# Kernel optimization log

Hardware: AMD Instinct MI355X
Metric: run time of the kernel (lower is better)

## Reference

```python
import jax, jax.numpy as jnp
import numpy as np

EPS = 1e-08
MOMENTUM_WEIGHT = 1.0
CONTINUITY_WEIGHT = 10.0
N = 192


def setup_inputs() -> dict:
    key = jax.random.key(0)
    k1, k2, k3, k4, k5, k6 = jax.random.split(key, 6)
    return {
        'u': jax.random.normal(k1, (N, N, N, 3), dtype=jnp.float32),
        'u_prev': jax.random.normal(k2, (N, N, N, 3), dtype=jnp.float32),
        'p': jax.random.normal(k3, (N, N, N), dtype=jnp.float32),
        'rho': jax.random.uniform(k4, (N, N, N), dtype=jnp.float32),
        'nu': jax.random.uniform(k5, (1,), dtype=jnp.float32),
        'h': jnp.ones((3,), dtype=jnp.float32),
        'dt': jnp.ones((1,), dtype=jnp.float32),
        'gravity': jnp.asarray([0.0, -9.81, 0.0], dtype=jnp.float32),
    }


def _central_diff(f, axis, h_ax):
    # (f[i+1] - f[i-1]) / (2h), periodic via roll (matches torch.roll)
    return (jnp.roll(f, -1, axis=axis) - jnp.roll(f, 1, axis=axis)) / (2.0 * h_ax)


def _laplacian(f, h):
    lap = jnp.zeros_like(f)
    for d in range(3):
        lap = lap + (jnp.roll(f, -1, axis=d) - 2.0 * f + jnp.roll(f, 1, axis=d)) / (h[d] ** 2)
    return lap


def reference(u, u_prev, p, rho, nu, h, dt, gravity):
    ux, uy, uz = u[..., 0], u[..., 1], u[..., 2]

    dux_dx = _central_diff(ux, 0, h[0]); dux_dy = _central_diff(ux, 1, h[1]); dux_dz = _central_diff(ux, 2, h[2])
    duy_dx = _central_diff(uy, 0, h[0]); duy_dy = _central_diff(uy, 1, h[1]); duy_dz = _central_diff(uy, 2, h[2])
    duz_dx = _central_diff(uz, 0, h[0]); duz_dy = _central_diff(uz, 1, h[1]); duz_dz = _central_diff(uz, 2, h[2])

    dp_dx = _central_diff(p, 0, h[0]); dp_dy = _central_diff(p, 1, h[1]); dp_dz = _central_diff(p, 2, h[2])

    lap_ux = _laplacian(ux, h); lap_uy = _laplacian(uy, h); lap_uz = _laplacian(uz, h)

    conv_x = ux * dux_dx + uy * dux_dy + uz * dux_dz
    conv_y = ux * duy_dx + uy * duy_dy + uz * duy_dz
    conv_z = ux * duz_dx + uy * duz_dy + uz * duz_dz

    # t > 0 branch: backward-difference time derivative
    dux_dt = (ux - u_prev[..., 0]) / dt[0]
    duy_dt = (uy - u_prev[..., 1]) / dt[0]
    duz_dt = (uz - u_prev[..., 2]) / dt[0]

    inv_rho = 1.0 / (rho + EPS)
    nu0 = nu[0]
    R_x = dux_dt + conv_x + dp_dx * inv_rho - nu0 * lap_ux - gravity[0]
    R_y = duy_dt + conv_y + dp_dy * inv_rho - nu0 * lap_uy - gravity[1]
    R_z = duz_dt + conv_z + dp_dz * inv_rho - nu0 * lap_uz - gravity[2]

    R_cont = dux_dx + duy_dy + duz_dz

    momentum_loss = (R_x ** 2 + R_y ** 2 + R_z ** 2).mean()
    continuity_loss = (R_cont ** 2).mean()
    total = MOMENTUM_WEIGHT * momentum_loss + CONTINUITY_WEIGHT * continuity_loss
    return jnp.stack([total, momentum_loss, continuity_loss])
```

## Files before the change

kernel.cpp:

```cpp
#include <hip/hip_runtime.h>

#define GN 192
#define GNN (GN * GN)
#define GTOT (GN * GN * GN)
#define NSLOTS 256
#define NT (GTOT / 2)
#define NBLK (NT / 256)
#define CHUNK (NBLK / 8)

typedef int   int32x4_t __attribute__((ext_vector_type(4)));
typedef float floatx4_t __attribute__((ext_vector_type(4)));
typedef float floatx2_t __attribute__((ext_vector_type(2)));
typedef float v2        __attribute__((ext_vector_type(2)));

extern "C" __device__ floatx4_t
llvm_amdgcn_raw_buffer_load_fp32x4(int32x4_t srsrc, int voffset, int soffset,
                                   int aux) __asm("llvm.amdgcn.raw.buffer.load.v4f32");
extern "C" __device__ floatx2_t
llvm_amdgcn_raw_buffer_load_fp32x2(int32x4_t srsrc, int voffset, int soffset,
                                   int aux) __asm("llvm.amdgcn.raw.buffer.load.v2f32");
extern "C" __device__ float
llvm_amdgcn_raw_buffer_load_fp32(int32x4_t srsrc, int voffset, int soffset,
                                 int aux) __asm("llvm.amdgcn.raw.buffer.load.f32");

__device__ __forceinline__ int32x4_t make_srd(const void* ptr, unsigned bytes) {
    int32x4_t r;
    unsigned long long a = (unsigned long long)ptr;
    r.x = (int)(unsigned)(a & 0xFFFFFFFFu);
    r.y = (int)(unsigned)(a >> 32);
    r.z = (int)bytes;
    r.w = 0x00020000;
    return r;
}

__global__ __launch_bounds__(256, 2) void ns_loss_kernel(
    const float* __restrict__ u,
    const float* __restrict__ uprev,
    const float* __restrict__ p,
    const float* __restrict__ rho,
    const float* __restrict__ nu,
    const float* __restrict__ h,
    const float* __restrict__ dt,
    const float* __restrict__ grav,
    double* __restrict__ acc)
{
    const int d = blockIdx.x;
    const int o = (d & 7) * CHUNK + (d >> 3);
    const int g = o * 256 + threadIdx.x;
    const int m  = g % 96;
    const int ln = g / 96;
    const int j  = ln % GN;
    const int i  = ln / GN;
    const int k0 = 2 * m;
    const int c0 = ln * GN + k0;
    const int c1 = c0 + 1;
    const int lane = threadIdx.x & 63;

    const int ipb = (i == GN-1) ? c0 - (GN - 1) * GNN : c0 + GNN;
    const int imb = (i == 0)    ? c0 + (GN - 1) * GNN : c0 - GNN;
    const int jpb = (j == GN-1) ? c0 - (GN - 1) * GN  : c0 + GN;
    const int jmb = (j == 0)    ? c0 + (GN - 1) * GN  : c0 - GN;

    const int32x4_t srd_u  = make_srd(u,     (unsigned)GTOT * 12u);
    const int32x4_t srd_up = make_srd(uprev, (unsigned)GTOT * 12u);
    const int32x4_t srd_p  = make_srd(p,     (unsigned)GTOT * 4u);
    const int32x4_t srd_r  = make_srd(rho,   (unsigned)GTOT * 4u);

    const floatx4_t B  = llvm_amdgcn_raw_buffer_load_fp32x4(srd_u, 12 * c0, 0, 0);
    const floatx4_t C2 = llvm_amdgcn_raw_buffer_load_fp32x4(srd_u, 12 * c0 + 16, 0, 0);
    const floatx4_t E1 = llvm_amdgcn_raw_buffer_load_fp32x4(srd_u, 12 * ipb, 0, 0);
    const floatx4_t E2 = llvm_amdgcn_raw_buffer_load_fp32x4(srd_u, 12 * ipb + 16, 0, 0);
    const floatx4_t G1 = llvm_amdgcn_raw_buffer_load_fp32x4(srd_u, 12 * imb, 0, 0);
    const floatx4_t G2 = llvm_amdgcn_raw_buffer_load_fp32x4(srd_u, 12 * imb + 16, 0, 0);
    const floatx4_t I1 = llvm_amdgcn_raw_buffer_load_fp32x4(srd_u, 12 * jpb, 0, 0);
    const floatx4_t I2 = llvm_amdgcn_raw_buffer_load_fp32x4(srd_u, 12 * jpb + 16, 0, 0);
    const floatx4_t K1 = llvm_amdgcn_raw_buffer_load_fp32x4(srd_u, 12 * jmb, 0, 0);
    const floatx4_t K2 = llvm_amdgcn_raw_buffer_load_fp32x4(srd_u, 12 * jmb + 16, 0, 0);
    const floatx4_t M  = llvm_amdgcn_raw_buffer_load_fp32x4(srd_up, 12 * c0, 0, 0);
    const floatx4_t M2 = llvm_amdgcn_raw_buffer_load_fp32x4(srd_up, 12 * c0 + 16, 0, 0);
    const floatx2_t P0  = llvm_amdgcn_raw_buffer_load_fp32x2(srd_p, 4 * c0, 0, 0);
    const floatx2_t Pip = llvm_amdgcn_raw_buffer_load_fp32x2(srd_p, 4 * ipb, 0, 0);
    const floatx2_t Pim = llvm_amdgcn_raw_buffer_load_fp32x2(srd_p, 4 * imb, 0, 0);
    const floatx2_t Pjp = llvm_amdgcn_raw_buffer_load_fp32x2(srd_p, 4 * jpb, 0, 0);
    const floatx2_t Pjm = llvm_amdgcn_raw_buffer_load_fp32x2(srd_p, 4 * jmb, 0, 0);
    const floatx2_t RR  = llvm_amdgcn_raw_buffer_load_fp32x2(srd_r, 4 * c0, 0, 0);

    const float h0 = h[0], h1v = h[1], h2v = h[2];
    const float i2h0 = 0.5f / h0, i2h1 = 0.5f / h1v, i2h2 = 0.5f / h2v;
    const float ihs0 = 1.0f / (h0 * h0), ihs1 = 1.0f / (h1v * h1v), ihs2 = 1.0f / (h2v * h2v);
    const float invdt = 1.0f / dt[0];
    const float nu0 = nu[0];
    const float g0 = grav[0], g1v = grav[1], g2v = grav[2];
    const float s2h = 2.0f * (ihs0 + ihs1 + ihs2);

    __builtin_amdgcn_sched_barrier(0);

    const float c0x = B.x,  c0y = B.y,  c0z = B.z;
    const float c1x = B.w,  c1y = C2.x, c1z = C2.y;

    v2 zmx = {__shfl_up(c1x, 1), c0x};
    v2 zmy = {__shfl_up(c1y, 1), c0y};
    v2 zmz = {__shfl_up(c1z, 1), c0z};
    v2 zpx = {c1x, __shfl_down(c0x, 1)};
    v2 zpy = {c1y, __shfl_down(c0y, 1)};
    v2 zpz = {c1z, __shfl_down(c0z, 1)};
    v2 pzm2 = {__shfl_up((float)P0.y, 1), P0.x};
    v2 pzp2 = {P0.y, __shfl_down((float)P0.x, 1)};

    if (m == 0 || lane == 0) {
        const int zmc = (m == 0) ? c0 + (GN - 1) : c0 - 1;
        const floatx4_t A = llvm_amdgcn_raw_buffer_load_fp32x4(srd_u, 12 * zmc, 0, 0);
        zmx.x = A.x; zmy.x = A.y; zmz.x = A.z;
        pzm2.x = llvm_amdgcn_raw_buffer_load_fp32(srd_p, 4 * zmc, 0, 0);
    }
    if (m == 95 || lane == 63) {
        const int zpc = (m == 95) ? c1 - (GN - 1) : c1 + 1;
        const floatx4_t D = llvm_amdgcn_raw_buffer_load_fp32x4(srd_u, 12 * zpc, 0, 0);
        zpx.y = D.x; zpy.y = D.y; zpz.y = D.z;
        pzp2.y = llvm_amdgcn_raw_buffer_load_fp32(srd_p, 4 * zpc, 0, 0);
    }

    const v2 ucx = {c0x, c1x}, ucy = {c0y, c1y}, ucz = {c0z, c1z};
    const v2 xpx = {E1.x, E1.w}, xpy = {E1.y, E2.x}, xpz = {E1.z, E2.y};
    const v2 xmx = {G1.x, G1.w}, xmy = {G1.y, G2.x}, xmz = {G1.z, G2.y};
    const v2 ypx = {I1.x, I1.w}, ypy = {I1.y, I2.x}, ypz = {I1.z, I2.y};
    const v2 ymx = {K1.x, K1.w}, ymy = {K1.y, K2.x}, ymz = {K1.z, K2.y};
    const v2 upx = {M.x, M.w},  upy = {M.y, M2.x}, upz = {M.z, M2.y};

    v2 dXx = (xpx - xmx) * i2h0, dXy = (xpy - xmy) * i2h0, dXz = (xpz - xmz) * i2h0;
    v2 dYx = (ypx - ymx) * i2h1, dYy = (ypy - ymy) * i2h1, dYz = (ypz - ymz) * i2h1;
    v2 dZx = (zpx - zmx) * i2h2, dZy = (zpy - zmy) * i2h2, dZz = (zpz - zmz) * i2h2;

    v2 lapx = (xpx + xmx) * ihs0 + (ypx + ymx) * ihs1 + (zpx + zmx) * ihs2 - ucx * s2h;
    v2 lapy = (xpy + xmy) * ihs0 + (ypy + ymy) * ihs1 + (zpy + zmy) * ihs2 - ucy * s2h;
    v2 lapz = (xpz + xmz) * ihs0 + (ypz + ymz) * ihs1 + (zpz + zmz) * ihs2 - ucz * s2h;

    v2 convx = ucx * dXx + ucy * dYx + ucz * dZx;
    v2 convy = ucx * dXy + ucy * dYy + ucz * dZy;
    v2 convz = ucx * dXz + ucy * dYz + ucz * dZz;

    v2 dpx = (Pip - Pim) * i2h0;
    v2 dpy = (Pjp - Pjm) * i2h1;
    v2 dpz = (pzp2 - pzm2) * i2h2;

    v2 irho;
    irho.x = __builtin_amdgcn_rcpf(RR.x + 1e-8f);
    irho.y = __builtin_amdgcn_rcpf(RR.y + 1e-8f);

    v2 Rx = (ucx - upx) * invdt + convx + dpx * irho - lapx * nu0 - g0;
    v2 Ry = (ucy - upy) * invdt + convy + dpy * irho - lapy * nu0 - g1v;
    v2 Rz = (ucz - upz) * invdt + convz + dpz * irho - lapz * nu0 - g2v;
    v2 Rc = dXx + dYy + dZz;

    v2 m2 = Rx * Rx + Ry * Ry + Rz * Rz;
    v2 c2 = Rc * Rc;
    float msum = m2.x + m2.y;
    float csum = c2.x + c2.y;

    #pragma unroll
    for (int off = 32; off > 0; off >>= 1) {
        msum += __shfl_down(msum, off);
        csum += __shfl_down(csum, off);
    }

    __shared__ double smom[4], scont[4];
    const int wid = threadIdx.x >> 6;
    if (lane == 0) { smom[wid] = (double)msum; scont[wid] = (double)csum; }
    __syncthreads();
    if (threadIdx.x == 0) {
        const double mm = smom[0] + smom[1] + smom[2] + smom[3];
        const double cc = scont[0] + scont[1] + scont[2] + scont[3];
        double* slot = acc + 2 * (blockIdx.x & (NSLOTS - 1));
        unsafeAtomicAdd(slot, mm);
        unsafeAtomicAdd(slot + 1, cc);
    }
}

__global__ __launch_bounds__(256) void ns_finalize_kernel(const double* __restrict__ acc,
                                                          float* __restrict__ out)
{
    const int tid = threadIdx.x;
    double mom = acc[2 * tid];
    double cont = acc[2 * tid + 1];
    #pragma unroll
    for (int off = 32; off > 0; off >>= 1) {
        mom  += __shfl_down(mom, off);
        cont += __shfl_down(cont, off);
    }
    __shared__ double smom[4], scont[4];
    const int wid = tid >> 6;
    const int lane = tid & 63;
    if (lane == 0) { smom[wid] = mom; scont[wid] = cont; }
    __syncthreads();
    if (tid == 0) {
        const double m = (smom[0] + smom[1] + smom[2] + smom[3]) / (double)GTOT;
        const double c = (scont[0] + scont[1] + scont[2] + scont[3]) / (double)GTOT;
        out[0] = (float)(m + 10.0 * c);
        out[1] = (float)m;
        out[2] = (float)c;
    }
}

extern "C" void kernel_launch(void* const* d_in, const int* in_sizes, int n_in,
                              void* d_out, int out_size, void* d_ws, size_t ws_size,
                              hipStream_t stream)
{
    const float* u     = (const float*)d_in[0];
    const float* uprev = (const float*)d_in[1];
    const float* p     = (const float*)d_in[2];
    const float* rho   = (const float*)d_in[3];
    const float* nu    = (const float*)d_in[4];
    const float* h     = (const float*)d_in[5];
    const float* dt    = (const float*)d_in[6];
    const float* grav  = (const float*)d_in[7];

    double* acc = (double*)d_ws;

    (void)hipMemsetAsync(d_ws, 0, NSLOTS * 2 * sizeof(double), stream);

    ns_loss_kernel<<<NBLK, 256, 0, stream>>>(u, uprev, p, rho, nu, h, dt, grav, acc);
    ns_finalize_kernel<<<1, 256, 0, stream>>>(acc, (float*)d_out);
}
```

Before: 49.78 us.

## Stage velocity rows in LDS per block covering two j-rows

Each block now handles one i-plane and two adjacent j-rows with 192 threads. It cooperatively loads the eight needed velocity rows (center, j±1, i±1) into shared memory with coalesced 16-byte loads, and every thread then reads its stencil neighbors from LDS. The aim is fewer redundant, poorly aligned global u loads and fewer per-thread vector loads. The cost is a block barrier, about 18KB of LDS per block, and a different block/occupancy configuration. Neighbor-row data is still fetched from global memory, so the total traffic reduction is limited.

```diff
diff --git a/kernel.cpp b/kernel.cpp
--- a/kernel.cpp
+++ b/kernel.cpp
@@ -4,8 +4,7 @@
 #define GNN (GN * GN)
 #define GTOT (GN * GN * GN)
 #define NSLOTS 256
-#define NT (GTOT / 2)
-#define NBLK (NT / 256)
+#define NBLK (GN * 96)
 #define CHUNK (NBLK / 8)
 
 typedef int   int32x4_t __attribute__((ext_vector_type(4)));
@@ -33,7 +32,7 @@
     return r;
 }
 
-__global__ __launch_bounds__(256, 2) void ns_loss_kernel(
+__global__ __launch_bounds__(192, 4) void ns_loss_kernel(
     const float* __restrict__ u,
     const float* __restrict__ uprev,
     const float* __restrict__ p,
@@ -44,46 +43,66 @@
     const float* __restrict__ grav,
     double* __restrict__ acc)
 {
+    __shared__ __align__(16) float ldsU[8 * 576];
+
     const int d = blockIdx.x;
     const int o = (d & 7) * CHUNK + (d >> 3);
-    const int g = o * 256 + threadIdx.x;
-    const int m  = g % 96;
-    const int ln = g / 96;
-    const int j  = ln % GN;
-    const int i  = ln / GN;
-    const int k0 = 2 * m;
-    const int c0 = ln * GN + k0;
-    const int c1 = c0 + 1;
-    const int lane = threadIdx.x & 63;
-
-    const int ipb = (i == GN-1) ? c0 - (GN - 1) * GNN : c0 + GNN;
-    const int imb = (i == 0)    ? c0 + (GN - 1) * GNN : c0 - GNN;
-    const int jpb = (j == GN-1) ? c0 - (GN - 1) * GN  : c0 + GN;
-    const int jmb = (j == 0)    ? c0 + (GN - 1) * GN  : c0 - GN;
+    const int i   = o / 96;
+    const int jpi = o % 96;
+    const int j0 = 2 * jpi, j1 = j0 + 1;
+    const int t = threadIdx.x;
+    const int lane = t & 63;
+
+    const int jmr = (j0 == 0)      ? GN - 1 : j0 - 1;
+    const int jpr = (j1 == GN - 1) ? 0      : j1 + 1;
+    const int imr = (i == 0)       ? GN - 1 : i - 1;
+    const int ipr = (i == GN - 1)  ? 0      : i + 1;
 
     const int32x4_t srd_u  = make_srd(u,     (unsigned)GTOT * 12u);
     const int32x4_t srd_up = make_srd(uprev, (unsigned)GTOT * 12u);
     const int32x4_t srd_p  = make_srd(p,     (unsigned)GTOT * 4u);
     const int32x4_t srd_r  = make_srd(rho,   (unsigned)GTOT * 4u);
 
-    const floatx4_t B  = llvm_amdgcn_raw_buffer_load_fp32x4(srd_u, 12 * c0, 0, 0);
-    const floatx4_t C2 = llvm_amdgcn_raw_buffer_load_fp32x4(srd_u, 12 * c0 + 16, 0, 0);
-    const floatx4_t E1 = llvm_amdgcn_raw_buffer_load_fp32x4(srd_u, 12 * ipb, 0, 0);
-    const floatx4_t E2 = llvm_amdgcn_raw_buffer_load_fp32x4(srd_u, 12 * ipb + 16, 0, 0);
-    const floatx4_t G1 = llvm_amdgcn_raw_buffer_load_fp32x4(srd_u, 12 * imb, 0, 0);
-    const floatx4_t G2 = llvm_amdgcn_raw_buffer_load_fp32x4(srd_u, 12 * imb + 16, 0, 0);
-    const floatx4_t I1 = llvm_amdgcn_raw_buffer_load_fp32x4(srd_u, 12 * jpb, 0, 0);
-    const floatx4_t I2 = llvm_amdgcn_raw_buffer_load_fp32x4(srd_u, 12 * jpb + 16, 0, 0);
-    const floatx4_t K1 = llvm_amdgcn_raw_buffer_load_fp32x4(srd_u, 12 * jmb, 0, 0);
-    const floatx4_t K2 = llvm_amdgcn_raw_buffer_load_fp32x4(srd_u, 12 * jmb + 16, 0, 0);
-    const floatx4_t M  = llvm_amdgcn_raw_buffer_load_fp32x4(srd_up, 12 * c0, 0, 0);
-    const floatx4_t M2 = llvm_amdgcn_raw_buffer_load_fp32x4(srd_up, 12 * c0 + 16, 0, 0);
-    const floatx2_t P0  = llvm_amdgcn_raw_buffer_load_fp32x2(srd_p, 4 * c0, 0, 0);
-    const floatx2_t Pip = llvm_amdgcn_raw_buffer_load_fp32x2(srd_p, 4 * ipb, 0, 0);
-    const floatx2_t Pim = llvm_amdgcn_raw_buffer_load_fp32x2(srd_p, 4 * imb, 0, 0);
-    const floatx2_t Pjp = llvm_amdgcn_raw_buffer_load_fp32x2(srd_p, 4 * jpb, 0, 0);
-    const floatx2_t Pjm = llvm_amdgcn_raw_buffer_load_fp32x2(srd_p, 4 * jmb, 0, 0);
-    const floatx2_t RR  = llvm_amdgcn_raw_buffer_load_fp32x2(srd_r, 4 * c0, 0, 0);
+    const int l   = t / 24;
+    const int sub = t - l * 24;
+    int srow, scol;
+    if (l < 4) { srow = i;                  scol = (l == 0) ? jmr : (l == 1) ? j0 : (l == 2) ? j1 : jpr; }
+    else       { srow = (l < 6) ? imr : ipr; scol = (l & 1) ? j1 : j0; }
+    const int gb = (srow * GN + scol) * GN;
+
+    const floatx4_t s0 = llvm_amdgcn_raw_buffer_load_fp32x4(srd_u, 12 * gb + 16 * (sub + 0),   0, 0);
+    const floatx4_t s1 = llvm_amdgcn_raw_buffer_load_fp32x4(srd_u, 12 * gb + 16 * (sub + 24),  0, 0);
+    const floatx4_t s2 = llvm_amdgcn_raw_buffer_load_fp32x4(srd_u, 12 * gb + 16 * (sub + 48),  0, 0);
+    const floatx4_t s3 = llvm_amdgcn_raw_buffer_load_fp32x4(srd_u, 12 * gb + 16 * (sub + 72),  0, 0);
+    const floatx4_t s4 = llvm_amdgcn_raw_buffer_load_fp32x4(srd_u, 12 * gb + 16 * (sub + 96),  0, 0);
+    const floatx4_t s5 = llvm_amdgcn_raw_buffer_load_fp32x4(srd_u, 12 * gb + 16 * (sub + 120), 0, 0);
+
+    const int jj = t / 96;
+    const int mm = t - jj * 96;
+    const int jr = j0 + jj;
+    const int k0 = 2 * mm;
+    const int c0g = (i * GN + jr) * GN + k0;
+    const int jrp = (jj == 0) ? j1 : jpr;
+    const int jrm = (jj == 0) ? jmr : j0;
+
+    const floatx4_t M  = llvm_amdgcn_raw_buffer_load_fp32x4(srd_up, 12 * c0g,      0, 0);
+    const floatx4_t M2 = llvm_amdgcn_raw_buffer_load_fp32x4(srd_up, 12 * c0g + 16, 0, 0);
+    const floatx2_t P0  = llvm_amdgcn_raw_buffer_load_fp32x2(srd_p, 4 * c0g, 0, 0);
+    const floatx2_t Pip = llvm_amdgcn_raw_buffer_load_fp32x2(srd_p, 4 * ((ipr * GN + jr) * GN + k0), 0, 0);
+    const floatx2_t Pim = llvm_amdgcn_raw_buffer_load_fp32x2(srd_p, 4 * ((imr * GN + jr) * GN + k0), 0, 0);
+    const floatx2_t Pjp = llvm_amdgcn_raw_buffer_load_fp32x2(srd_p, 4 * ((i * GN + jrp) * GN + k0), 0, 0);
+    const floatx2_t Pjm = llvm_amdgcn_raw_buffer_load_fp32x2(srd_p, 4 * ((i * GN + jrm) * GN + k0), 0, 0);
+    const floatx2_t RR  = llvm_amdgcn_raw_buffer_load_fp32x2(srd_r, 4 * c0g, 0, 0);
+
+    {
+        const int wb = l * 576 + 4 * sub;
+        *(floatx4_t*)&ldsU[wb]           = s0;
+        *(floatx4_t*)&ldsU[wb + 4 * 24]  = s1;
+        *(floatx4_t*)&ldsU[wb + 4 * 48]  = s2;
+        *(floatx4_t*)&ldsU[wb + 4 * 72]  = s3;
+        *(floatx4_t*)&ldsU[wb + 4 * 96]  = s4;
+        *(floatx4_t*)&ldsU[wb + 4 * 120] = s5;
+    }
 
     const float h0 = h[0], h1v = h[1], h2v = h[2];
     const float i2h0 = 0.5f / h0, i2h1 = 0.5f / h1v, i2h2 = 0.5f / h2v;
@@ -93,10 +112,33 @@
     const float g0 = grav[0], g1v = grav[1], g2v = grav[2];
     const float s2h = 2.0f * (ihs0 + ihs1 + ihs2);
 
-    __builtin_amdgcn_sched_barrier(0);
-
-    const float c0x = B.x,  c0y = B.y,  c0z = B.z;
-    const float c1x = B.w,  c1y = C2.x, c1z = C2.y;
+    __syncthreads();
+
+    const int lc  = 1 + jj;
+    const int ljm = jj ? 1 : 0;
+    const int ljp = jj ? 3 : 2;
+    const int lim = 4 + jj;
+    const int lip = 6 + jj;
+    const int dwc = 6 * mm;
+
+    #define RD6(L, X, Y, Z)                                              \
+        v2 X, Y, Z;                                                      \
+        {                                                                \
+            const v2 r0 = *(const v2*)&ldsU[(L) * 576 + dwc];            \
+            const v2 r1 = *(const v2*)&ldsU[(L) * 576 + dwc + 2];        \
+            const v2 r2 = *(const v2*)&ldsU[(L) * 576 + dwc + 4];        \
+            X = v2{r0.x, r1.y}; Y = v2{r0.y, r2.x}; Z = v2{r1.x, r2.y};  \
+        }
+
+    RD6(lc,  ucx, ucy, ucz)
+    RD6(ljm, ymx, ymy, ymz)
+    RD6(ljp, ypx, ypy, ypz)
+    RD6(lim, xmx, xmy, xmz)
+    RD6(lip, xpx, xpy, xpz)
+    #undef RD6
+
+    const float c0x = ucx.x, c0y = ucy.x, c0z = ucz.x;
+    const float c1x = ucx.y, c1y = ucy.y, c1z = ucz.y;
 
     v2 zmx = {__shfl_up(c1x, 1), c0x};
     v2 zmy = {__shfl_up(c1y, 1), c0y};
@@ -107,25 +149,22 @@
     v2 pzm2 = {__shfl_up((float)P0.y, 1), P0.x};
     v2 pzp2 = {P0.y, __shfl_down((float)P0.x, 1)};
 
-    if (m == 0 || lane == 0) {
-        const int zmc = (m == 0) ? c0 + (GN - 1) : c0 - 1;
-        const floatx4_t A = llvm_amdgcn_raw_buffer_load_fp32x4(srd_u, 12 * zmc, 0, 0);
-        zmx.x = A.x; zmy.x = A.y; zmz.x = A.z;
-        pzm2.x = llvm_amdgcn_raw_buffer_load_fp32(srd_p, 4 * zmc, 0, 0);
-    }
-    if (m == 95 || lane == 63) {
-        const int zpc = (m == 95) ? c1 - (GN - 1) : c1 + 1;
-        const floatx4_t D = llvm_amdgcn_raw_buffer_load_fp32x4(srd_u, 12 * zpc, 0, 0);
-        zpx.y = D.x; zpy.y = D.y; zpz.y = D.z;
-        pzp2.y = llvm_amdgcn_raw_buffer_load_fp32(srd_p, 4 * zpc, 0, 0);
-    }
-
-    const v2 ucx = {c0x, c1x}, ucy = {c0y, c1y}, ucz = {c0z, c1z};
-    const v2 xpx = {E1.x, E1.w}, xpy = {E1.y, E2.x}, xpz = {E1.z, E2.y};
-    const v2 xmx = {G1.x, G1.w}, xmy = {G1.y, G2.x}, xmz = {G1.z, G2.y};
-    const v2 ypx = {I1.x, I1.w}, ypy = {I1.y, I2.x}, ypz = {I1.z, I2.y};
-    const v2 ymx = {K1.x, K1.w}, ymy = {K1.y, K2.x}, ymz = {K1.z, K2.y};
-    const v2 upx = {M.x, M.w},  upy = {M.y, M2.x}, upz = {M.z, M2.y};
+    if (mm == 0 || lane == 0) {
+        const int km = (k0 + GN - 1) % GN;
+        const int dw = lc * 576 + 3 * km;
+        zmx.x = ldsU[dw]; zmy.x = ldsU[dw + 1]; zmz.x = ldsU[dw + 2];
+        const int zmc_g = (mm == 0) ? c0g + (GN - 1) : c0g - 1;
+        pzm2.x = llvm_amdgcn_raw_buffer_load_fp32(srd_p, 4 * zmc_g, 0, 0);
+    }
+    if (mm == 95 || lane == 63) {
+        const int kp = (k0 + 2) % GN;
+        const int dw = lc * 576 + 3 * kp;
+        zpx.y = ldsU[dw]; zpy.y = ldsU[dw + 1]; zpz.y = ldsU[dw + 2];
+        const int zpc_g = (mm == 95) ? c0g + 2 - GN : c0g + 2;
+        pzp2.y = llvm_amdgcn_raw_buffer_load_fp32(srd_p, 4 * zpc_g, 0, 0);
+    }
+
+    const v2 upx = {M.x, M.w}, upy = {M.y, M2.x}, upz = {M.z, M2.y};
 
     v2 dXx = (xpx - xmx) * i2h0, dXy = (xpy - xmy) * i2h0, dXz = (xpz - xmz) * i2h0;
     v2 dYx = (ypx - ymx) * i2h1, dYy = (ypy - ymy) * i2h1, dYz = (ypz - ymz) * i2h1;
@@ -163,16 +202,16 @@
         csum += __shfl_down(csum, off);
     }
 
-    __shared__ double smom[4], scont[4];
-    const int wid = threadIdx.x >> 6;
+    __shared__ double smom[3], scont[3];
+    const int wid = t >> 6;
     if (lane == 0) { smom[wid] = (double)msum; scont[wid] = (double)csum; }
     __syncthreads();
-    if (threadIdx.x == 0) {
-        const double mm = smom[0] + smom[1] + smom[2] + smom[3];
-        const double cc = scont[0] + scont[1] + scont[2] + scont[3];
+    if (t == 0) {
+        const double mmv = smom[0] + smom[1] + smom[2];
+        const double ccv = scont[0] + scont[1] + scont[2];
         double* slot = acc + 2 * (blockIdx.x & (NSLOTS - 1));
-        unsafeAtomicAdd(slot, mm);
-        unsafeAtomicAdd(slot + 1, cc);
+        unsafeAtomicAdd(slot, mmv);
+        unsafeAtomicAdd(slot + 1, ccv);
     }
 }
 
@@ -218,6 +257,6 @@
 
     (void)hipMemsetAsync(d_ws, 0, NSLOTS * 2 * sizeof(double), stream);
 
-    ns_loss_kernel<<<NBLK, 256, 0, stream>>>(u, uprev, p, rho, nu, h, dt, grav, acc);
+    ns_loss_kernel<<<NBLK, 192, 0, stream>>>(u, uprev, p, rho, nu, h, dt, grav, acc);
     ns_finalize_kernel<<<1, 256, 0, stream>>>(acc, (float*)d_out);
 }
```

Measured after the change: 50.76 us. About the same (+2.0%).
